# Kernel optimization log

Hardware: AMD Instinct MI355X
Metric: run time of the kernel (lower is better)

## Reference

```python
import jax, jax.numpy as jnp
import numpy as np

P = 2          # number of additive secret shares (2-party)
B = 2          # batch
S = 1024       # seq_len
D = 1024       # hidden_size
H = 16         # num_attention_heads
HD = D // H    # attention_head_size = 64
MASK_VAL = -10000.0


def setup_inputs() -> dict:
    key = jax.random.key(0)
    ks = jax.random.split(key, 6)
    w_scale = 0.02
    return {
        "hidden_shares": jax.random.normal(ks[0], (P, B, S, D), jnp.float32),
        "attention_mask": jnp.ones((B, S), jnp.float32),
        "wq": jax.random.normal(ks[1], (D, D), jnp.float32) * w_scale,
        "bq": jnp.zeros((D,), jnp.float32),
        "wk": jax.random.normal(ks[2], (D, D), jnp.float32) * w_scale,
        "bk": jnp.zeros((D,), jnp.float32),
        "wv": jax.random.normal(ks[3], (D, D), jnp.float32) * w_scale,
        "bv": jnp.zeros((D,), jnp.float32),
        "wo": jax.random.normal(ks[4], (D, D), jnp.float32) * w_scale,
        "bo": jnp.zeros((D,), jnp.float32),
    }


def reference(hidden_shares, attention_mask, wq, bq, wk, bk, wv, bv, wo, bo):
    """Secret-shared multi-head attention. Values are carried as P additive
    shares (leading axis); interactive protocol ops (matmul, softmax) are
    modeled as reconstruct -> compute -> reshare with fresh correlated masks,
    which is exactly the plaintext semantics the MPC protocol realizes."""
    scale = np.float32(1.0 / np.sqrt(HD))
    base = jax.random.key(42)  # protocol PRG for resharing masks

    def recon(x):  # [P, ...] -> [...]
        return x.sum(0)

    def reshare(v, tag):  # value -> P additive shares summing to v
        m = jax.random.normal(jax.random.fold_in(base, tag), v.shape, v.dtype) * 0.1
        return jnp.stack([v - m, m])

    def secure_linear(x_sh, w, b, tag):  # torch Linear: x @ w.T + b
        return reshare(recon(x_sh) @ w.T + b, tag)

    def split_heads(x_sh):  # [P,B,S,D] -> [P,B,H,S,HD] (per-share reshape/permute)
        return x_sh.reshape(P, B, S, H, HD).transpose(0, 1, 3, 2, 4)

    q = split_heads(secure_linear(hidden_shares, wq, bq, 0))
    k = split_heads(secure_linear(hidden_shares, wk, bk, 1))
    v = split_heads(secure_linear(hidden_shares, wv, bv, 2))

    # secure QK^T (matmul via reconstruct/reshare), then public scalar scale per-share
    scores = reshare(jnp.einsum('bhsd,bhtd->bhst', recon(q), recon(k)), 3) * scale

    # additive mask, shared, then share-wise secure_add
    additive = (1.0 - attention_mask)[:, None, None, :] * MASK_VAL  # [B,1,1,S]
    scores = scores + reshare(additive, 4)

    probs = reshare(jax.nn.softmax(recon(scores), axis=-1), 5)
    ctx = reshare(jnp.einsum('bhst,bhtd->bhsd', recon(probs), recon(v)), 6)

    # transpose back from scores: [P,B,H,S,HD] -> [P,B,S,D]
    ctx = ctx.transpose(0, 1, 3, 2, 4).reshape(P, B, S, D)

    out = secure_linear(ctx, wo, bo, 7)
    return recon(out)  # reconstructed output [B, S, D]
```

## Files before the change

kernel.cpp:

```cpp
#include <hip/hip_runtime.h>
#include <hip/hip_bf16.h>

#define BB 2
#define SS 1024
#define DD 1024
#define HH 16
#define HDD 64
#define MASK_VAL -10000.0f
#define LOG2E 1.44269504f
#define BSD (BB * SS * DD)

typedef __attribute__((ext_vector_type(8))) short bf16x8;
typedef __attribute__((ext_vector_type(4))) short short4v;
typedef __attribute__((ext_vector_type(4))) float f32x4;
typedef __attribute__((ext_vector_type(16))) float f32x16;
typedef __attribute__((ext_vector_type(4))) unsigned int uint4v;

__device__ __forceinline__ short f2bf(float f) {
    union { float f; unsigned u; } v; v.f = f;
    unsigned r = v.u + 0x7FFFu + ((v.u >> 16) & 1u);
    return (short)(r >> 16);
}
__device__ __forceinline__ float bf2f(short s) {
    union { unsigned u; float f; } v;
    v.u = ((unsigned)(unsigned short)s) << 16;
    return v.f;
}
__device__ __forceinline__ unsigned cvt_pk_bf16(float lo, float hi) {
    unsigned r;
    asm("v_cvt_pk_bf16_f32 %0, %1, %2" : "=v"(r) : "v"(lo), "v"(hi));
    return r;
}
__device__ __forceinline__ float v_exp2(float x) {
    float r;
    asm("v_exp_f32 %0, %1" : "=v"(r) : "v"(x));
    return r;
}
__device__ __forceinline__ void plane32_swap(unsigned& a, unsigned& b) {
#if __has_builtin(__builtin_amdgcn_permlane32_swap)
    auto r = __builtin_amdgcn_permlane32_swap(a, b, false, false);
    a = r[0]; b = r[1];
#else
    unsigned as = (unsigned)__shfl_xor((int)a, 32);
    unsigned bs = (unsigned)__shfl_xor((int)b, 32);
    bool lo = ((threadIdx.x & 63) < 32);
    unsigned na = lo ? a : bs;
    unsigned nb = lo ? as : b;
    a = na; b = nb;
#endif
}

__global__ __launch_bounds__(256) void k_prep(
    const float* __restrict__ h,
    const float* __restrict__ wq, const float* __restrict__ wk,
    const float* __restrict__ wv, const float* __restrict__ wo,
    short* __restrict__ xbf, short* __restrict__ wbf) {
    int id = blockIdx.x;
    if (id < 1024) {
        int i = id * 256 + threadIdx.x;
        const float4* h0 = (const float4*)h;
        const float4* h1 = (const float4*)(h + (size_t)BSD);
        float4 a0 = h0[2 * i], a1 = h0[2 * i + 1];
        float4 b0 = h1[2 * i], b1 = h1[2 * i + 1];
        bf16x8 o;
        o[0] = f2bf(a0.x + b0.x); o[1] = f2bf(a0.y + b0.y);
        o[2] = f2bf(a0.z + b0.z); o[3] = f2bf(a0.w + b0.w);
        o[4] = f2bf(a1.x + b1.x); o[5] = f2bf(a1.y + b1.y);
        o[6] = f2bf(a1.z + b1.z); o[7] = f2bf(a1.w + b1.w);
        ((bf16x8*)xbf)[i] = o;
    } else {
        int zi = (id - 1024) >> 9;
        int i = ((id - 1024) & 511) * 256 + threadIdx.x;
        const float* src = (zi == 0) ? wq : (zi == 1) ? wk : (zi == 2) ? wv : wo;
        short* dst = wbf + (size_t)zi * (DD * DD);
        const float4* s4 = (const float4*)src;
        float4 a0 = s4[2 * i], a1 = s4[2 * i + 1];
        bf16x8 o;
        o[0] = f2bf(a0.x); o[1] = f2bf(a0.y); o[2] = f2bf(a0.z); o[3] = f2bf(a0.w);
        o[4] = f2bf(a1.x); o[5] = f2bf(a1.y); o[6] = f2bf(a1.z); o[7] = f2bf(a1.w);
        ((bf16x8*)dst)[i] = o;
    }
}

#define QBM 128
#define QBN 64
#define QBK 64

__global__ __launch_bounds__(256) void k_gemm_qkv(
    const short* __restrict__ xbf, const short* __restrict__ wbf,
    const float* __restrict__ bq, const float* __restrict__ bk,
    const float* __restrict__ bv,
    short* __restrict__ qb, short* __restrict__ kb, short* __restrict__ vt) {
    __shared__ __align__(16) short As[QBM * QBK];
    __shared__ __align__(16) short Bs[QBN * QBK];
    const int z = blockIdx.z;
    const short* W = wbf + (size_t)z * (DD * DD);
    const float* bias = (z == 0) ? bq : (z == 1) ? bk : bv;
    const int bm = blockIdx.y * QBM;
    const int bn = blockIdx.x * QBN;
    const int tid = threadIdx.x;
    const int lane = tid & 63;
    const int wid = tid >> 6;
    const int wm = wid >> 1;
    const int wn = wid & 1;
    const int lr = lane & 15;
    const int kq = lane >> 4;

    f32x4 acc[4][2];
#pragma unroll
    for (int i = 0; i < 4; ++i)
#pragma unroll
        for (int j = 0; j < 2; ++j) acc[i][j] = (f32x4)0.0f;

    for (int k0 = 0; k0 < DD; k0 += QBK) {
#pragma unroll
        for (int i = 0; i < 4; ++i) {
            int s = i * 256 + tid;
            int r = s >> 3;
            int cs = (s & 7) ^ (r & 7);
            __builtin_amdgcn_global_load_lds(
                (const __attribute__((address_space(1))) unsigned*)(xbf + (size_t)(bm + r) * DD + k0 + (cs << 3)),
                (__attribute__((address_space(3))) unsigned*)&As[s * 8], 16, 0, 0);
        }
#pragma unroll
        for (int i = 0; i < 2; ++i) {
            int s = i * 256 + tid;
            int r = s >> 3;
            int cs = (s & 7) ^ (r & 7);
            __builtin_amdgcn_global_load_lds(
                (const __attribute__((address_space(1))) unsigned*)(W + (size_t)(bn + r) * DD + k0 + (cs << 3)),
                (__attribute__((address_space(3))) unsigned*)&Bs[s * 8], 16, 0, 0);
        }
        __syncthreads();

        bf16x8 af[4][2], bfr[2][2];
#pragma unroll
        for (int f = 0; f < 4; ++f) {
            int row = wm * 64 + f * 16 + lr;
#pragma unroll
            for (int ks = 0; ks < 2; ++ks) {
                int cpos = ((ks << 2) | kq) ^ (row & 7);
                af[f][ks] = *(const bf16x8*)&As[row * QBK + (cpos << 3)];
            }
        }
#pragma unroll
        for (int g = 0; g < 2; ++g) {
            int row = wn * 32 + g * 16 + lr;
#pragma unroll
            for (int ks = 0; ks < 2; ++ks) {
                int cpos = ((ks << 2) | kq) ^ (row & 7);
                bfr[g][ks] = *(const bf16x8*)&Bs[row * QBK + (cpos << 3)];
            }
        }
#pragma unroll
        for (int fm = 0; fm < 4; ++fm)
#pragma unroll
            for (int fn = 0; fn < 2; ++fn)
#pragma unroll
                for (int ks = 0; ks < 2; ++ks)
                    acc[fm][fn] = __builtin_amdgcn_mfma_f32_16x16x32_bf16(
                        af[fm][ks], bfr[fn][ks], acc[fm][fn], 0, 0, 0);
        __syncthreads();
    }

    if (z < 2) {
        short* C = (z == 0) ? qb : kb;
#pragma unroll
        for (int fm = 0; fm < 4; ++fm) {
            int row0 = bm + wm * 64 + fm * 16 + kq * 4;
#pragma unroll
            for (int fn = 0; fn < 2; ++fn) {
                int col = bn + wn * 32 + fn * 16 + lr;
                float bv_ = bias[col];
#pragma unroll
                for (int j = 0; j < 4; ++j)
                    C[(size_t)(row0 + j) * DD + col] = f2bf(acc[fm][fn][j] + bv_);
            }
        }
    } else {
#pragma unroll
        for (int fm = 0; fm < 4; ++fm) {
            int row0 = bm + wm * 64 + fm * 16 + kq * 4;
            int bidx = row0 >> 10, s0 = row0 & 1023;
#pragma unroll
            for (int fn = 0; fn < 2; ++fn) {
                int col = bn + wn * 32 + fn * 16 + lr;
                float bv_ = bias[col];
                size_t addr = ((size_t)(bidx * HH + (col >> 6)) * HDD + (col & 63)) * SS + s0;
                short4v o;
                o.x = f2bf(acc[fm][fn][0] + bv_); o.y = f2bf(acc[fm][fn][1] + bv_);
                o.z = f2bf(acc[fm][fn][2] + bv_); o.w = f2bf(acc[fm][fn][3] + bv_);
                *(short4v*)&vt[addr] = o;
            }
        }
    }
}

#define OM 64
#define ON 64
#define OK 64

__global__ __launch_bounds__(256) void k_gemm_out(
    const short* __restrict__ A, const short* __restrict__ W,
    const float* __restrict__ bias, float* __restrict__ C) {
    __shared__ __align__(16) short As[OM * OK];
    __shared__ __align__(16) short Bs[ON * OK];
    const int bm = blockIdx.y * OM;
    const int bn = blockIdx.x * ON;
    const int tid = threadIdx.x;
    const int lane = tid & 63;
    const int wid = tid >> 6;
    const int wm = wid & 1;
    const int wn = wid >> 1;
    const int lr = lane & 15;
    const int kq = lane >> 4;

    f32x4 acc[2][2];
#pragma unroll
    for (int i = 0; i < 2; ++i)
#pragma unroll
        for (int j = 0; j < 2; ++j) acc[i][j] = (f32x4)0.0f;

    for (int k0 = 0; k0 < DD; k0 += OK) {
#pragma unroll
        for (int i = 0; i < 2; ++i) {
            int t2 = i * 256 + tid;
            int r = t2 >> 3;
            int cs = (t2 & 7) ^ (r & 7);
            __builtin_amdgcn_global_load_lds(
                (const __attribute__((address_space(1))) unsigned*)(A + (size_t)(bm + r) * DD + k0 + (cs << 3)),
                (__attribute__((address_space(3))) unsigned*)&As[t2 * 8], 16, 0, 0);
        }
#pragma unroll
        for (int i = 0; i < 2; ++i) {
            int t2 = i * 256 + tid;
            int r = t2 >> 3;
            int cs = (t2 & 7) ^ (r & 7);
            __builtin_amdgcn_global_load_lds(
                (const __attribute__((address_space(1))) unsigned*)(W + (size_t)(bn + r) * DD + k0 + (cs << 3)),
                (__attribute__((address_space(3))) unsigned*)&Bs[t2 * 8], 16, 0, 0);
        }
        __syncthreads();

        bf16x8 af[2][2], bfr[2][2];
#pragma unroll
        for (int f = 0; f < 2; ++f) {
            int rowa = wm * 32 + f * 16 + lr;
            int rowb = wn * 32 + f * 16 + lr;
#pragma unroll
            for (int ks = 0; ks < 2; ++ks) {
                int ca = (((ks << 2) | kq)) ^ (rowa & 7);
                int cb = (((ks << 2) | kq)) ^ (rowb & 7);
                af[f][ks] = *(const bf16x8*)&As[rowa * OK + (ca << 3)];
                bfr[f][ks] = *(const bf16x8*)&Bs[rowb * OK + (cb << 3)];
            }
        }
#pragma unroll
        for (int fm = 0; fm < 2; ++fm)
#pragma unroll
            for (int fn = 0; fn < 2; ++fn)
#pragma unroll
                for (int ks = 0; ks < 2; ++ks)
                    acc[fm][fn] = __builtin_amdgcn_mfma_f32_16x16x32_bf16(
                        af[fm][ks], bfr[fn][ks], acc[fm][fn], 0, 0, 0);
        __syncthreads();
    }

#pragma unroll
    for (int fm = 0; fm < 2; ++fm) {
        int row0 = bm + wm * 32 + fm * 16 + kq * 4;
#pragma unroll
        for (int fn = 0; fn < 2; ++fn) {
            int col = bn + wn * 32 + fn * 16 + lr;
            float bv_ = bias[col];
#pragma unroll
            for (int j = 0; j < 4; ++j)
                C[(size_t)(row0 + j) * DD + col] = acc[fm][fn][j] + bv_;
        }
    }
}

__global__ __launch_bounds__(256) void k_attn(
    const short* __restrict__ qb, const short* __restrict__ kb,
    const short* __restrict__ vt, const float* __restrict__ mask,
    short* __restrict__ ctx) {
    __shared__ __align__(16) short Kls[2][2][64 * 64];
    __shared__ __align__(16) short Vls[2][2][64 * 64];

    const int bh = blockIdx.x;
    const int b = bh >> 4;
    const int h = bh & 15;
    const int q0 = blockIdx.y << 6;
    const int tid = threadIdx.x;
    const int gtid = tid & 127;
    const int kvh = tid >> 7;
    const int lane = tid & 63;
    const int w4 = (tid >> 6) & 1;
    const int ql = lane & 31;
    const int hi = lane >> 5;
    const int rsw = ql & 7;
    const int tbase = kvh << 9;
    const float scale2 = 0.125f * LOG2E;
    const float mval2 = MASK_VAL * LOG2E;

    const short* khead = kb + (size_t)b * SS * DD + h * HDD;
    const short* vhead = vt + (size_t)bh * HDD * SS;
    const float* maskp = mask + b * SS;

    bf16x8 qf0, qf1, qf2, qf3;
    {
        const short* qrow = qb + ((size_t)(b * SS + q0 + w4 * 32 + ql)) * DD + h * HDD + hi * 8;
        qf0 = *(const bf16x8*)(qrow);
        qf1 = *(const bf16x8*)(qrow + 16);
        qf2 = *(const bf16x8*)(qrow + 32);
        qf3 = *(const bf16x8*)(qrow + 48);
    }

    auto stage = [&](int t0, int bi) {
        const short* kbase = khead + (size_t)t0 * DD;
        const short* vbase = vhead + t0;
#pragma unroll
        for (int i = 0; i < 4; ++i) {
            int t = i * 128 + gtid;
            int r = t >> 3;
            int cs = (t & 7) ^ (r & 7);
            __builtin_amdgcn_global_load_lds(
                (const __attribute__((address_space(1))) unsigned*)(kbase + (size_t)r * DD + cs * 8),
                (__attribute__((address_space(3))) unsigned*)&Kls[kvh][bi][t * 8], 16, 0, 0);
        }
#pragma unroll
        for (int i = 0; i < 4; ++i) {
            int t = i * 128 + gtid;
            int r = t >> 3;
            int cs = (t & 7) ^ (r & 7);
            __builtin_amdgcn_global_load_lds(
                (const __attribute__((address_space(1))) unsigned*)(vbase + (size_t)r * SS + cs * 8),
                (__attribute__((address_space(3))) unsigned*)&Vls[kvh][bi][t * 8], 16, 0, 0);
        }
    };

    float m_r = -3.0e38f, l_r = 0.0f;
    f32x16 O0 = (f32x16)0.0f, O1 = (f32x16)0.0f;

    auto body = [&](int t0, int cur, int tail) {
        const short* Kb = &Kls[kvh][cur][0];
        const short* Vb = &Vls[kvh][cur][0];

        f32x16 s0 = (f32x16)0.0f, s1 = (f32x16)0.0f;
        __builtin_amdgcn_s_setprio(1);
#pragma unroll
        for (int step = 0; step < 4; ++step) {
            int cpos = ((step << 1) | hi) ^ rsw;
            bf16x8 k0 = *(const bf16x8*)&Kb[ql * 64 + (cpos << 3)];
            bf16x8 k1 = *(const bf16x8*)&Kb[(32 + ql) * 64 + (cpos << 3)];
            bf16x8 qf = (step == 0) ? qf0 : (step == 1) ? qf1 : (step == 2) ? qf2 : qf3;
            s0 = __builtin_amdgcn_mfma_f32_32x32x16_bf16(k0, qf, s0, 0, 0, 0);
            s1 = __builtin_amdgcn_mfma_f32_32x32x16_bf16(k1, qf, s1, 0, 0, 0);
        }
        __builtin_amdgcn_s_setprio(0);

#pragma unroll
        for (int g = 0; g < 4; ++g) {
            float4 a4 = *(const float4*)&maskp[t0 + 8 * g + 4 * hi];
            float4 b4 = *(const float4*)&maskp[t0 + 32 + 8 * g + 4 * hi];
            s0[4 * g + 0] = fmaf(s0[4 * g + 0], scale2, (1.0f - a4.x) * mval2);
            s0[4 * g + 1] = fmaf(s0[4 * g + 1], scale2, (1.0f - a4.y) * mval2);
            s0[4 * g + 2] = fmaf(s0[4 * g + 2], scale2, (1.0f - a4.z) * mval2);
            s0[4 * g + 3] = fmaf(s0[4 * g + 3], scale2, (1.0f - a4.w) * mval2);
            s1[4 * g + 0] = fmaf(s1[4 * g + 0], scale2, (1.0f - b4.x) * mval2);
            s1[4 * g + 1] = fmaf(s1[4 * g + 1], scale2, (1.0f - b4.y) * mval2);
            s1[4 * g + 2] = fmaf(s1[4 * g + 2], scale2, (1.0f - b4.z) * mval2);
            s1[4 * g + 3] = fmaf(s1[4 * g + 3], scale2, (1.0f - b4.w) * mval2);
        }

        float mt[16];
#pragma unroll
        for (int r = 0; r < 16; ++r) mt[r] = fmaxf(s0[r], s1[r]);
#pragma unroll
        for (int st = 8; st > 0; st >>= 1)
#pragma unroll
            for (int r = 0; r < 8; ++r)
                if (r < st) mt[r] = fmaxf(mt[r], mt[r + st]);
        float mx = fmaxf(mt[0], __shfl_xor(mt[0], 32));

        bool need = mx > m_r + 8.0f;
        if (__any(need)) {
            float mn = fmaxf(m_r, mx);
            float alpha = v_exp2(m_r - mn);
            m_r = mn;
            l_r *= alpha;
#pragma unroll
            for (int r = 0; r < 16; ++r) {
                int qrow = (r & 3) + 8 * (r >> 2) + 4 * hi;
                float al = __shfl(alpha, qrow, 64);
                O0[r] *= al;
                O1[r] *= al;
            }
        }

        float st0[16];
#pragma unroll
        for (int r = 0; r < 16; ++r) {
            s0[r] = v_exp2(s0[r] - m_r);
            s1[r] = v_exp2(s1[r] - m_r);
            st0[r] = s0[r] + s1[r];
        }
#pragma unroll
        for (int st = 8; st > 0; st >>= 1)
#pragma unroll
            for (int r = 0; r < 8; ++r)
                if (r < st) st0[r] += st0[r + st];
        l_r += st0[0] + __shfl_xor(st0[0], 32);

        unsigned w0 = cvt_pk_bf16(s0[0], s0[1]),  w1 = cvt_pk_bf16(s0[2], s0[3]);
        unsigned w2 = cvt_pk_bf16(s0[4], s0[5]),  w3 = cvt_pk_bf16(s0[6], s0[7]);
        unsigned w4_ = cvt_pk_bf16(s0[8], s0[9]),  w5 = cvt_pk_bf16(s0[10], s0[11]);
        unsigned w6 = cvt_pk_bf16(s0[12], s0[13]), w7 = cvt_pk_bf16(s0[14], s0[15]);
        plane32_swap(w0, w2); plane32_swap(w1, w3);
        plane32_swap(w4_, w6); plane32_swap(w5, w7);
        uint4v f0 = {w0, w1, w2, w3};
        uint4v f1 = {w4_, w5, w6, w7};
        unsigned x0 = cvt_pk_bf16(s1[0], s1[1]),  x1 = cvt_pk_bf16(s1[2], s1[3]);
        unsigned x2 = cvt_pk_bf16(s1[4], s1[5]),  x3 = cvt_pk_bf16(s1[6], s1[7]);
        unsigned x4 = cvt_pk_bf16(s1[8], s1[9]),  x5 = cvt_pk_bf16(s1[10], s1[11]);
        unsigned x6 = cvt_pk_bf16(s1[12], s1[13]), x7 = cvt_pk_bf16(s1[14], s1[15]);
        plane32_swap(x0, x2); plane32_swap(x1, x3);
        plane32_swap(x4, x6); plane32_swap(x5, x7);
        uint4v f2 = {x0, x1, x2, x3};
        uint4v f3 = {x4, x5, x6, x7};

        bf16x8 pf0 = __builtin_bit_cast(bf16x8, f0);
        bf16x8 pf1 = __builtin_bit_cast(bf16x8, f1);
        bf16x8 pf2 = __builtin_bit_cast(bf16x8, f2);
        bf16x8 pf3 = __builtin_bit_cast(bf16x8, f3);

        if (tail) { asm volatile("s_waitcnt vmcnt(0)\n\ts_barrier" ::: "memory"); }
        else      { asm volatile("s_waitcnt vmcnt(8)\n\ts_barrier" ::: "memory"); }

        __builtin_amdgcn_s_setprio(1);
#pragma unroll
        for (int ks = 0; ks < 4; ++ks) {
            int cpos = ((ks << 1) | hi) ^ rsw;
            bf16x8 pf = (ks == 0) ? pf0 : (ks == 1) ? pf1 : (ks == 2) ? pf2 : pf3;
            bf16x8 v0 = *(const bf16x8*)&Vb[ql * 64 + (cpos << 3)];
            bf16x8 v1 = *(const bf16x8*)&Vb[(32 + ql) * 64 + (cpos << 3)];
            O0 = __builtin_amdgcn_mfma_f32_32x32x16_bf16(pf, v0, O0, 0, 0, 0);
            O1 = __builtin_amdgcn_mfma_f32_32x32x16_bf16(pf, v1, O1, 0, 0, 0);
        }
        __builtin_amdgcn_s_setprio(0);
    };

    stage(tbase, 0);
    for (int it = 0; it < 7; ++it) {
        stage(tbase + ((it + 1) << 6), (it + 1) & 1);
        asm volatile("s_waitcnt vmcnt(12)\n\ts_barrier" ::: "memory");
        body(tbase + (it << 6), it & 1, 0);
        asm volatile("s_barrier" ::: "memory");
    }
    asm volatile("s_waitcnt vmcnt(4)\n\ts_barrier" ::: "memory");
    body(tbase + (7 << 6), 1, 1);

    __syncthreads();
    float* osh = (float*)&Kls[0][0][0];
    float* mlsh = (float*)&Vls[0][0][0];
    if (kvh == 1) {
        float* obuf = osh + w4 * 2048;
#pragma unroll
        for (int r = 0; r < 16; ++r) {
            int qrow = (r & 3) + 8 * (r >> 2) + 4 * hi;
            obuf[qrow * 64 + ql] = O0[r];
            obuf[qrow * 64 + 32 + ql] = O1[r];
        }
        if (lane < 32) {
            mlsh[w4 * 64 + ql] = m_r;
            mlsh[w4 * 64 + 32 + ql] = l_r;
        }
    }
    __syncthreads();
    if (kvh == 0) {
        float* obuf = osh + w4 * 2048;
        float m2 = mlsh[w4 * 64 + ql];
        float l2 = mlsh[w4 * 64 + 32 + ql];
        float m = fmaxf(m_r, m2);
        float a1 = v_exp2(m_r - m), a2 = v_exp2(m2 - m);
        float inv = 1.0f / (l_r * a1 + l2 * a2);
        float c1 = a1 * inv, c2 = a2 * inv;
        short* cb = ctx + ((size_t)(b * SS + q0 + w4 * 32)) * DD + h * HDD;
#pragma unroll
        for (int r = 0; r < 16; ++r) {
            int qrow = (r & 3) + 8 * (r >> 2) + 4 * hi;
            float cc1 = __shfl(c1, qrow, 64);
            float cc2 = __shfl(c2, qrow, 64);
            float ob0 = obuf[qrow * 64 + ql];
            float ob1 = obuf[qrow * 64 + 32 + ql];
            cb[(size_t)qrow * DD + ql]      = f2bf(O0[r] * cc1 + ob0 * cc2);
            cb[(size_t)qrow * DD + 32 + ql] = f2bf(O1[r] * cc1 + ob1 * cc2);
        }
    }
}

extern "C" void kernel_launch(void* const* d_in, const int* in_sizes, int n_in,
                              void* d_out, int out_size, void* d_ws, size_t ws_size,
                              hipStream_t stream) {
    const float* h    = (const float*)d_in[0];
    const float* mask = (const float*)d_in[1];
    const float* wq   = (const float*)d_in[2];
    const float* bq   = (const float*)d_in[3];
    const float* wk   = (const float*)d_in[4];
    const float* bk   = (const float*)d_in[5];
    const float* wv   = (const float*)d_in[6];
    const float* bv   = (const float*)d_in[7];
    const float* wo   = (const float*)d_in[8];
    const float* bo   = (const float*)d_in[9];
    float* out = (float*)d_out;

    char* base = (char*)d_ws;
    short* x_bf  = (short*)base;
    short* w_bf  = (short*)(base + (4u << 20));
    short* q_bf  = (short*)(base + (12u << 20));
    short* k_bf  = (short*)(base + (16u << 20));
    short* v_t   = (short*)(base + (20u << 20));
    short* ctxbf = (short*)(base + (24u << 20));

    k_prep<<<3072, 256, 0, stream>>>(h, wq, wk, wv, wo, x_bf, w_bf);

    dim3 gqkv(DD / QBN, BB * SS / QBM, 3);
    k_gemm_qkv<<<gqkv, 256, 0, stream>>>(x_bf, w_bf, bq, bk, bv, q_bf, k_bf, v_t);

    dim3 gattn(BB * HH, SS / 64);
    k_attn<<<gattn, 256, 0, stream>>>(q_bf, k_bf, v_t, mask, ctxbf);

    dim3 gout(DD / ON, BB * SS / OM);
    k_gemm_out<<<gout, 256, 0, stream>>>(ctxbf, w_bf + (size_t)3 * DD * DD, bo, out);
}
```

Measured before the change: 63.56 us.

## Split attention KV range four ways across 512-thread blocks, drop double buffering

The attention kernel now splits each query tile's key/value range across four 128-thread groups instead of two, with 512 threads per block. Each group covers 256 keys in four iterations using a single K/V buffer, replacing the double-buffered prefetch pipeline with a load, full wait and barrier per iteration. The final merge combines four partial softmax states (max, sum, output) through shared memory instead of two. The aim is more waves in flight and a shorter serial loop per wave. The cost is that global loads no longer overlap with the MFMA work, more block-wide barriers, and a heavier four-way reduction at the end.

After: 68.47 us. 7.7% more time.

```diff
diff --git a/kernel.cpp b/kernel.cpp
--- a/kernel.cpp
+++ b/kernel.cpp
@@ -280,12 +280,11 @@
     }
 }
 
-__global__ __launch_bounds__(256) void k_attn(
+__global__ __launch_bounds__(512) void k_attn(
     const short* __restrict__ qb, const short* __restrict__ kb,
     const short* __restrict__ vt, const float* __restrict__ mask,
     short* __restrict__ ctx) {
-    __shared__ __align__(16) short Kls[2][2][64 * 64];
-    __shared__ __align__(16) short Vls[2][2][64 * 64];
+    __shared__ __align__(16) short KVls[8][64 * 64];
 
     const int bh = blockIdx.x;
     const int b = bh >> 4;
@@ -299,13 +298,15 @@
     const int ql = lane & 31;
     const int hi = lane >> 5;
     const int rsw = ql & 7;
-    const int tbase = kvh << 9;
+    const int tbase = kvh << 8;
     const float scale2 = 0.125f * LOG2E;
     const float mval2 = MASK_VAL * LOG2E;
 
     const short* khead = kb + (size_t)b * SS * DD + h * HDD;
     const short* vhead = vt + (size_t)bh * HDD * SS;
     const float* maskp = mask + b * SS;
+    short* Kbuf = &KVls[kvh * 2 + 0][0];
+    short* Vbuf = &KVls[kvh * 2 + 1][0];
 
     bf16x8 qf0, qf1, qf2, qf3;
     {
@@ -316,7 +317,7 @@
         qf3 = *(const bf16x8*)(qrow + 48);
     }
 
-    auto stage = [&](int t0, int bi) {
+    auto stage = [&](int t0) {
         const short* kbase = khead + (size_t)t0 * DD;
         const short* vbase = vhead + t0;
 #pragma unroll
@@ -326,7 +327,7 @@
             int cs = (t & 7) ^ (r & 7);
             __builtin_amdgcn_global_load_lds(
                 (const __attribute__((address_space(1))) unsigned*)(kbase + (size_t)r * DD + cs * 8),
-                (__attribute__((address_space(3))) unsigned*)&Kls[kvh][bi][t * 8], 16, 0, 0);
+                (__attribute__((address_space(3))) unsigned*)&Kbuf[t * 8], 16, 0, 0);
         }
 #pragma unroll
         for (int i = 0; i < 4; ++i) {
@@ -335,16 +336,16 @@
             int cs = (t & 7) ^ (r & 7);
             __builtin_amdgcn_global_load_lds(
                 (const __attribute__((address_space(1))) unsigned*)(vbase + (size_t)r * SS + cs * 8),
-                (__attribute__((address_space(3))) unsigned*)&Vls[kvh][bi][t * 8], 16, 0, 0);
+                (__attribute__((address_space(3))) unsigned*)&Vbuf[t * 8], 16, 0, 0);
         }
     };
 
     float m_r = -3.0e38f, l_r = 0.0f;
     f32x16 O0 = (f32x16)0.0f, O1 = (f32x16)0.0f;
 
-    auto body = [&](int t0, int cur, int tail) {
-        const short* Kb = &Kls[kvh][cur][0];
-        const short* Vb = &Vls[kvh][cur][0];
+    auto body = [&](int t0) {
+        const short* Kb = Kbuf;
+        const short* Vb = Vbuf;
 
         f32x16 s0 = (f32x16)0.0f, s1 = (f32x16)0.0f;
         __builtin_amdgcn_s_setprio(1);
@@ -412,14 +413,14 @@
                 if (r < st) st0[r] += st0[r + st];
         l_r += st0[0] + __shfl_xor(st0[0], 32);
 
-        unsigned w0 = cvt_pk_bf16(s0[0], s0[1]),  w1 = cvt_pk_bf16(s0[2], s0[3]);
-        unsigned w2 = cvt_pk_bf16(s0[4], s0[5]),  w3 = cvt_pk_bf16(s0[6], s0[7]);
-        unsigned w4_ = cvt_pk_bf16(s0[8], s0[9]),  w5 = cvt_pk_bf16(s0[10], s0[11]);
-        unsigned w6 = cvt_pk_bf16(s0[12], s0[13]), w7 = cvt_pk_bf16(s0[14], s0[15]);
-        plane32_swap(w0, w2); plane32_swap(w1, w3);
-        plane32_swap(w4_, w6); plane32_swap(w5, w7);
-        uint4v f0 = {w0, w1, w2, w3};
-        uint4v f1 = {w4_, w5, w6, w7};
+        unsigned pw0 = cvt_pk_bf16(s0[0], s0[1]),  pw1 = cvt_pk_bf16(s0[2], s0[3]);
+        unsigned pw2 = cvt_pk_bf16(s0[4], s0[5]),  pw3 = cvt_pk_bf16(s0[6], s0[7]);
+        unsigned pw4 = cvt_pk_bf16(s0[8], s0[9]),  pw5 = cvt_pk_bf16(s0[10], s0[11]);
+        unsigned pw6 = cvt_pk_bf16(s0[12], s0[13]), pw7 = cvt_pk_bf16(s0[14], s0[15]);
+        plane32_swap(pw0, pw2); plane32_swap(pw1, pw3);
+        plane32_swap(pw4, pw6); plane32_swap(pw5, pw7);
+        uint4v f0 = {pw0, pw1, pw2, pw3};
+        uint4v f1 = {pw4, pw5, pw6, pw7};
         unsigned x0 = cvt_pk_bf16(s1[0], s1[1]),  x1 = cvt_pk_bf16(s1[2], s1[3]);
         unsigned x2 = cvt_pk_bf16(s1[4], s1[5]),  x3 = cvt_pk_bf16(s1[6], s1[7]);
         unsigned x4 = cvt_pk_bf16(s1[8], s1[9]),  x5 = cvt_pk_bf16(s1[10], s1[11]);
@@ -434,9 +435,6 @@
         bf16x8 pf2 = __builtin_bit_cast(bf16x8, f2);
         bf16x8 pf3 = __builtin_bit_cast(bf16x8, f3);
 
-        if (tail) { asm volatile("s_waitcnt vmcnt(0)\n\ts_barrier" ::: "memory"); }
-        else      { asm volatile("s_waitcnt vmcnt(8)\n\ts_barrier" ::: "memory"); }
-
         __builtin_amdgcn_s_setprio(1);
 #pragma unroll
         for (int ks = 0; ks < 4; ++ks) {
@@ -450,21 +448,18 @@
         __builtin_amdgcn_s_setprio(0);
     };
 
-    stage(tbase, 0);
-    for (int it = 0; it < 7; ++it) {
-        stage(tbase + ((it + 1) << 6), (it + 1) & 1);
-        asm volatile("s_waitcnt vmcnt(12)\n\ts_barrier" ::: "memory");
-        body(tbase + (it << 6), it & 1, 0);
-        asm volatile("s_barrier" ::: "memory");
-    }
-    asm volatile("s_waitcnt vmcnt(4)\n\ts_barrier" ::: "memory");
-    body(tbase + (7 << 6), 1, 1);
-
-    __syncthreads();
-    float* osh = (float*)&Kls[0][0][0];
-    float* mlsh = (float*)&Vls[0][0][0];
-    if (kvh == 1) {
-        float* obuf = osh + w4 * 2048;
+#pragma unroll 1
+    for (int it = 0; it < 4; ++it) {
+        stage(tbase + (it << 6));
+        asm volatile("s_waitcnt vmcnt(0)\n\ts_barrier" ::: "memory");
+        body(tbase + (it << 6));
+        __builtin_amdgcn_s_barrier();
+    }
+
+    float* osh = (float*)&KVls[0][0];
+    float* mlsh = osh + 12288;
+    if (kvh != 0) {
+        float* obuf = osh + (((kvh - 1) << 1) + w4) * 2048;
 #pragma unroll
         for (int r = 0; r < 16; ++r) {
             int qrow = (r & 3) + 8 * (r >> 2) + 4 * hi;
@@ -472,29 +467,40 @@
             obuf[qrow * 64 + 32 + ql] = O1[r];
         }
         if (lane < 32) {
-            mlsh[w4 * 64 + ql] = m_r;
-            mlsh[w4 * 64 + 32 + ql] = l_r;
+            mlsh[((kvh - 1) << 7) + (w4 << 6) + ql] = m_r;
+            mlsh[((kvh - 1) << 7) + (w4 << 6) + 32 + ql] = l_r;
         }
     }
     __syncthreads();
     if (kvh == 0) {
-        float* obuf = osh + w4 * 2048;
-        float m2 = mlsh[w4 * 64 + ql];
-        float l2 = mlsh[w4 * 64 + 32 + ql];
-        float m = fmaxf(m_r, m2);
-        float a1 = v_exp2(m_r - m), a2 = v_exp2(m2 - m);
-        float inv = 1.0f / (l_r * a1 + l2 * a2);
-        float c1 = a1 * inv, c2 = a2 * inv;
+        float mm[3], ll[3];
+#pragma unroll
+        for (int g = 0; g < 3; ++g) {
+            mm[g] = mlsh[(g << 7) + (w4 << 6) + ql];
+            ll[g] = mlsh[(g << 7) + (w4 << 6) + 32 + ql];
+        }
+        float m = fmaxf(fmaxf(m_r, mm[0]), fmaxf(mm[1], mm[2]));
+        float a0 = v_exp2(m_r - m);
+        float a1 = v_exp2(mm[0] - m), a2 = v_exp2(mm[1] - m), a3 = v_exp2(mm[2] - m);
+        float inv = 1.0f / (l_r * a0 + ll[0] * a1 + ll[1] * a2 + ll[2] * a3);
+        float c0 = a0 * inv, c1 = a1 * inv, c2 = a2 * inv, c3 = a3 * inv;
+        float* ob1 = osh + (0 * 2 + w4) * 2048;
+        float* ob2 = osh + (1 * 2 + w4) * 2048;
+        float* ob3 = osh + (2 * 2 + w4) * 2048;
         short* cb = ctx + ((size_t)(b * SS + q0 + w4 * 32)) * DD + h * HDD;
 #pragma unroll
         for (int r = 0; r < 16; ++r) {
             int qrow = (r & 3) + 8 * (r >> 2) + 4 * hi;
+            float cc0 = __shfl(c0, qrow, 64);
             float cc1 = __shfl(c1, qrow, 64);
             float cc2 = __shfl(c2, qrow, 64);
-            float ob0 = obuf[qrow * 64 + ql];
-            float ob1 = obuf[qrow * 64 + 32 + ql];
-            cb[(size_t)qrow * DD + ql]      = f2bf(O0[r] * cc1 + ob0 * cc2);
-            cb[(size_t)qrow * DD + 32 + ql] = f2bf(O1[r] * cc1 + ob1 * cc2);
+            float cc3 = __shfl(c3, qrow, 64);
+            float lo = O0[r] * cc0 + ob1[qrow * 64 + ql] * cc1
+                     + ob2[qrow * 64 + ql] * cc2 + ob3[qrow * 64 + ql] * cc3;
+            float hi_ = O1[r] * cc0 + ob1[qrow * 64 + 32 + ql] * cc1
+                      + ob2[qrow * 64 + 32 + ql] * cc2 + ob3[qrow * 64 + 32 + ql] * cc3;
+            cb[(size_t)qrow * DD + ql]      = f2bf(lo);
+            cb[(size_t)qrow * DD + 32 + ql] = f2bf(hi_);
         }
     }
 }
@@ -528,7 +534,7 @@
     k_gemm_qkv<<<gqkv, 256, 0, stream>>>(x_bf, w_bf, bq, bk, bv, q_bf, k_bf, v_t);
 
     dim3 gattn(BB * HH, SS / 64);
-    k_attn<<<gattn, 256, 0, stream>>>(q_bf, k_bf, v_t, mask, ctxbf);
+    k_attn<<<gattn, 512, 0, stream>>>(q_bf, k_bf, v_t, mask, ctxbf);
 
     dim3 gout(DD / ON, BB * SS / OM);
     k_gemm_out<<<gout, 256, 0, stream>>>(ctxbf, w_bf + (size_t)3 * DD * DD, bo, out);
```

## Single-buffer V tiles in attention kernel, staging next V after PV

Applied to the files above, without the earlier changes.

Keeps K double-buffered but cuts V to one LDS buffer per KV half, staging the next V tile only after the current PV step finishes. This halves V shared memory, which may allow more resident blocks per CU. The cost is that the V load for the next tile now has only the following QK^T and softmax phase to hide behind, and the old mid-body wait before PV is folded into the loop-top barrier.

Result: no change. 62.70 us, median of 2 (-1.3%).

```diff
diff --git a/kernel.cpp b/kernel.cpp
--- a/kernel.cpp
+++ b/kernel.cpp
@@ -285,7 +285,7 @@
     const short* __restrict__ vt, const float* __restrict__ mask,
     short* __restrict__ ctx) {
     __shared__ __align__(16) short Kls[2][2][64 * 64];
-    __shared__ __align__(16) short Vls[2][2][64 * 64];
+    __shared__ __align__(16) short Vls[2][64 * 64];
 
     const int bh = blockIdx.x;
     const int b = bh >> 4;
@@ -316,9 +316,8 @@
         qf3 = *(const bf16x8*)(qrow + 48);
     }
 
-    auto stage = [&](int t0, int bi) {
+    auto stageK = [&](int t0, int bi) {
         const short* kbase = khead + (size_t)t0 * DD;
-        const short* vbase = vhead + t0;
 #pragma unroll
         for (int i = 0; i < 4; ++i) {
             int t = i * 128 + gtid;
@@ -328,6 +327,9 @@
                 (const __attribute__((address_space(1))) unsigned*)(kbase + (size_t)r * DD + cs * 8),
                 (__attribute__((address_space(3))) unsigned*)&Kls[kvh][bi][t * 8], 16, 0, 0);
         }
+    };
+    auto stageV = [&](int t0) {
+        const short* vbase = vhead + t0;
 #pragma unroll
         for (int i = 0; i < 4; ++i) {
             int t = i * 128 + gtid;
@@ -335,16 +337,16 @@
             int cs = (t & 7) ^ (r & 7);
             __builtin_amdgcn_global_load_lds(
                 (const __attribute__((address_space(1))) unsigned*)(vbase + (size_t)r * SS + cs * 8),
-                (__attribute__((address_space(3))) unsigned*)&Vls[kvh][bi][t * 8], 16, 0, 0);
+                (__attribute__((address_space(3))) unsigned*)&Vls[kvh][t * 8], 16, 0, 0);
         }
     };
 
     float m_r = -3.0e38f, l_r = 0.0f;
     f32x16 O0 = (f32x16)0.0f, O1 = (f32x16)0.0f;
 
-    auto body = [&](int t0, int cur, int tail) {
+    auto body = [&](int t0, int cur) {
         const short* Kb = &Kls[kvh][cur][0];
-        const short* Vb = &Vls[kvh][cur][0];
+        const short* Vb = &Vls[kvh][0];
 
         f32x16 s0 = (f32x16)0.0f, s1 = (f32x16)0.0f;
         __builtin_amdgcn_s_setprio(1);
@@ -434,9 +436,6 @@
         bf16x8 pf2 = __builtin_bit_cast(bf16x8, f2);
         bf16x8 pf3 = __builtin_bit_cast(bf16x8, f3);
 
-        if (tail) { asm volatile("s_waitcnt vmcnt(0)\n\ts_barrier" ::: "memory"); }
-        else      { asm volatile("s_waitcnt vmcnt(8)\n\ts_barrier" ::: "memory"); }
-
         __builtin_amdgcn_s_setprio(1);
 #pragma unroll
         for (int ks = 0; ks < 4; ++ks) {
@@ -450,19 +449,24 @@
         __builtin_amdgcn_s_setprio(0);
     };
 
-    stage(tbase, 0);
-    for (int it = 0; it < 7; ++it) {
-        stage(tbase + ((it + 1) << 6), (it + 1) & 1);
-        asm volatile("s_waitcnt vmcnt(12)\n\ts_barrier" ::: "memory");
-        body(tbase + (it << 6), it & 1, 0);
-        asm volatile("s_barrier" ::: "memory");
-    }
-    asm volatile("s_waitcnt vmcnt(4)\n\ts_barrier" ::: "memory");
-    body(tbase + (7 << 6), 1, 1);
+    stageK(tbase, 0);
+    stageV(tbase);
+#pragma unroll 1
+    for (int it = 0; it < 8; ++it) {
+        if (it < 7) {
+            stageK(tbase + ((it + 1) << 6), (it + 1) & 1);
+            asm volatile("s_waitcnt vmcnt(4)\n\ts_barrier" ::: "memory");
+        } else {
+            asm volatile("s_waitcnt vmcnt(0)\n\ts_barrier" ::: "memory");
+        }
+        body(tbase + (it << 6), it & 1);
+        __builtin_amdgcn_s_barrier();
+        if (it < 7) stageV(tbase + ((it + 1) << 6));
+    }
 
     __syncthreads();
     float* osh = (float*)&Kls[0][0][0];
-    float* mlsh = (float*)&Vls[0][0][0];
+    float* mlsh = (float*)&Vls[0][0];
     if (kvh == 1) {
         float* obuf = osh + w4 * 2048;
 #pragma unroll
```
